# Kernel optimization log

Hardware: AMD Instinct MI355X
Metric: run time of the kernel (lower is better)

## Reference

```python
import jax, jax.numpy as jnp
import numpy as np

EPS = 1e-5  # torch LayerNorm default

def _ln(x):
    # LayerNorm over last dim, no affine (elementwise_affine=False)
    m = jnp.mean(x, axis=-1, keepdims=True)
    v = jnp.var(x, axis=-1, keepdims=True)
    return (x - m) / jnp.sqrt(v + EPS)

def _build_orthogonal(phi):
    """Orthogonal matrix of the 'X' RBS circuit on d qubits (unary subspace).
    phi has 2d-3 angles: a descending diagonal of d-1 adjacent Givens rotations
    followed by an ascending diagonal of d-2. Each RBS(theta) acts on coords
    (k, k+1) as [[cos, sin], [-sin, cos]]."""
    d = (phi.shape[0] + 3) // 2
    W = jnp.eye(d, dtype=phi.dtype)
    wires = list(range(d - 1)) + list(range(d - 3, -1, -1))  # 2d-3 gates
    for g, k in enumerate(wires):
        c, s = jnp.cos(phi[g]), jnp.sin(phi[g])
        rk, rk1 = W[k], W[k + 1]
        W = W.at[k].set(c * rk + s * rk1)
        W = W.at[k + 1].set(-s * rk + c * rk1)
    return W

def setup_inputs() -> dict:
    key = jax.random.key(0)
    ks = jax.random.split(key, 8)
    B, N, E, H, dh = 16, 1024, 512, 8, 64
    return {
        "x": jax.random.normal(ks[0], (B, N, E), jnp.float32),
        "Wv": jax.random.normal(ks[1], (H, dh, dh), jnp.float32) / np.sqrt(dh).astype(np.float32),
        "bv": jnp.zeros((H, dh), jnp.float32),
        "phi": jax.random.uniform(ks[2], (H, 2 * dh - 3), jnp.float32, 0.0, 2.0 * np.pi),
        "W1": jax.random.normal(ks[3], (E, E), jnp.float32) / np.sqrt(E).astype(np.float32),
        "b1": jnp.zeros((E,), jnp.float32),
        "W2": jax.random.normal(ks[4], (E, E), jnp.float32) / np.sqrt(E).astype(np.float32),
        "b2": jnp.zeros((E,), jnp.float32),
    }

def reference(x, Wv, bv, phi, W1, b1, W2, b2):
    B, N, E = x.shape
    H = Wv.shape[0]
    dh = E // H
    xn = _ln(x)                                    # norm1
    xh = xn.reshape(B, N, H, dh)                   # per-head slices
    Worth = jax.vmap(_build_orthogonal)(phi)       # [H, dh, dh]
    # per-head value projection (nn.Linear weights stored as [in, out])
    V = jnp.einsum('bnhd,hde->bnhe', xh, Wv) + bv  # [B,N,H,dh]
    # quantum attention scores: loader(x_j) -> W(phi) -> inverse loader(x_i),
    # rescaled by |x_i||x_j|  ==  A_ij = x_i^T W(phi) x_j
    A = jnp.einsum('bnhd,hde,bmhe->bhnm', xh, Worth, xh)
    P = jax.nn.softmax(A / np.float32(np.sqrt(dh)), axis=-1)
    attn = jnp.einsum('bhnm,bmhe->bnhe', P, V)
    head_out = _ln(attn + xh)                      # per-head LN over dh
    res = head_out.reshape(B, N, E) + x            # MHA + residual
    # merger: Linear -> GELU(exact) -> Linear on norm2(res)
    h = jax.nn.gelu(_ln(res) @ W1 + b1, approximate=False) @ W2 + b2
    return h + res
```

## Files before the change

### kernel.cpp

```cpp
#include <hip/hip_runtime.h>
#include <hip/hip_bf16.h>
#include <math.h>

#define B_  16
#define N_  1024
#define E_  512
#define H_  8

typedef __attribute__((ext_vector_type(8)))  __bf16 bf16x8;
typedef __attribute__((ext_vector_type(4)))  float  f32x4;
typedef __attribute__((ext_vector_type(16))) float  f32x16;
typedef __attribute__((ext_vector_type(4)))  unsigned int u32x4;

struct alignas(16) bf8pack { __hip_bfloat16 v[8]; };
struct alignas(8)  bf4pack { __hip_bfloat16 v[4]; };

static __device__ __forceinline__ float bf2f(__hip_bfloat16 x) { return __bfloat162float(x); }
static __device__ __forceinline__ __hip_bfloat16 f2bf(float x) { return __float2bfloat16(x); }

static __device__ __forceinline__ unsigned pkbf(float lo, float hi) {
    unsigned r;
    asm("v_cvt_pk_bf16_f32 %0, %1, %2" : "=v"(r) : "v"(lo), "v"(hi));
    return r;
}
static __device__ __forceinline__ void swap32(unsigned &a, unsigned &b) {
    asm("v_permlane32_swap_b32 %0, %1" : "+v"(a), "+v"(b));
}
static __device__ __forceinline__ void gload16(const __hip_bfloat16* g, __hip_bfloat16* l) {
    __builtin_amdgcn_global_load_lds(
        (const __attribute__((address_space(1))) unsigned*)g,
        (__attribute__((address_space(3))) unsigned*)l, 16, 0, 0);
}
#define MFMA32(a, b, c) __builtin_amdgcn_mfma_f32_32x32x16_bf16((a), (b), (c), 0, 0, 0)
#define MFMA16(a, b, c) __builtin_amdgcn_mfma_f32_16x16x32_bf16((a), (b), (c), 0, 0, 0)

static __device__ __forceinline__ float gelu_f(float v) {
    float z = fabsf(v) * 0.70710678118654752f;
    float t = 1.0f / fmaf(0.3275911f, z, 1.0f);
    float p = t * fmaf(t, fmaf(t, fmaf(t, fmaf(t, 1.061405429f, -1.453152027f),
                                       1.421413741f), -0.284496736f), 0.254829592f);
    float e = __builtin_amdgcn_exp2f(-z * z * 1.4426950408889634f);
    float erf = 1.0f - p * e;
    erf = copysignf(erf, v);
    return 0.5f * v * (1.0f + erf);
}

__global__ __launch_bounds__(256) void k_prep(const float* __restrict__ phi,
                                              const float* __restrict__ Wv,
                                              const float* __restrict__ W1,
                                              const float* __restrict__ W2,
                                              __hip_bfloat16* __restrict__ worth_t,
                                              __hip_bfloat16* __restrict__ wvt,
                                              __hip_bfloat16* __restrict__ w1t,
                                              __hip_bfloat16* __restrict__ w2t,
                                              float* __restrict__ csum1) {
    __shared__ float sh[64 * 65];
    int tid = threadIdx.x;
    if (blockIdx.x < 128) {
        int bid = blockIdx.x;
        const float* src = (bid & 1) ? W2 : W1;
        __hip_bfloat16* dst = (bid & 1) ? w2t : w1t;
        int tile = bid >> 1;
        int i0 = (tile & 7) * 64, o0 = (tile >> 3) * 64;
        float (*ts)[65] = (float(*)[65])sh;
        int r = tid >> 4, c4 = (tid & 15) * 4;
#pragma unroll
        for (int j4 = 0; j4 < 4; ++j4) {
            float4 v = *reinterpret_cast<const float4*>(&src[(size_t)(i0 + r + 16 * j4) * 512 + o0 + c4]);
            ts[r + 16 * j4][c4 + 0] = v.x; ts[r + 16 * j4][c4 + 1] = v.y;
            ts[r + 16 * j4][c4 + 2] = v.z; ts[r + 16 * j4][c4 + 3] = v.w;
        }
        __syncthreads();
        int o = tid >> 3, cg = tid & 7;
#pragma unroll
        for (int half = 0; half < 2; ++half) {
            int oo = o + 32 * half;
            bf8pack p;
#pragma unroll
            for (int j = 0; j < 8; ++j) p.v[j] = f2bf(ts[cg * 8 + j][oo]);
            *reinterpret_cast<bf8pack*>(&dst[(size_t)(o0 + oo) * 512 + i0 + cg * 8]) = p;
        }
    } else if (blockIdx.x < 136) {
        const float SCL = 0.18033688011112042f;
        int h = blockIdx.x - 128;
        int t = tid;
        if (t < 64) {
            for (int i = 0; i < 64; ++i) sh[i * 65 + t] = (i == t) ? 1.0f : 0.0f;
            for (int g = 0; g < 125; ++g) {
                int k = (g < 63) ? g : (124 - g);
                float ph = phi[h * 125 + g];
                float c, s;
                __sincosf(ph, &s, &c);
                float a  = sh[k * 65 + t];
                float b  = sh[(k + 1) * 65 + t];
                sh[k * 65 + t]       =  c * a + s * b;
                sh[(k + 1) * 65 + t] = -s * a + c * b;
            }
            for (int d = 0; d < 64; ++d)
                worth_t[h * 4096 + t * 64 + d] = f2bf(sh[d * 65 + t] * SCL);
            for (int d = 0; d < 64; ++d)
                wvt[h * 4096 + t * 64 + d] = f2bf(Wv[h * 4096 + d * 64 + t]);
        }
    } else {
        int c0 = (blockIdx.x - 136) * 64;
        float (*acc)[68] = (float(*)[68])sh;
        int cg = (tid & 15) * 4, rg = tid >> 4;
        float4 s4 = {0.f, 0.f, 0.f, 0.f};
        for (int rr = 0; rr < 32; ++rr) {
            float4 v = *reinterpret_cast<const float4*>(&W1[(size_t)(rg * 32 + rr) * 512 + c0 + cg]);
            s4.x += v.x; s4.y += v.y; s4.z += v.z; s4.w += v.w;
        }
        acc[rg][cg + 0] = s4.x; acc[rg][cg + 1] = s4.y;
        acc[rg][cg + 2] = s4.z; acc[rg][cg + 3] = s4.w;
        __syncthreads();
        if (tid < 64) {
            float s = 0.f;
#pragma unroll
            for (int g = 0; g < 16; ++g) s += acc[g][tid];
            csum1[c0 + tid] = s;
        }
    }
}

__global__ __launch_bounds__(256) void k_ln1(const float* __restrict__ in,
                                             __hip_bfloat16* __restrict__ out,
                                             __hip_bfloat16* __restrict__ outx) {
    int w = threadIdx.x >> 6, l = threadIdx.x & 63;
    size_t row = (size_t)blockIdx.x * 4 + w;
    const float* p = in + row * 512 + l * 8;
    float4 v0 = *reinterpret_cast<const float4*>(p);
    float4 v1 = *reinterpret_cast<const float4*>(p + 4);
    float vv[8] = {v0.x, v0.y, v0.z, v0.w, v1.x, v1.y, v1.z, v1.w};
    bf8pack xo;
#pragma unroll
    for (int j = 0; j < 8; ++j) xo.v[j] = f2bf(vv[j]);
    *reinterpret_cast<bf8pack*>(outx + row * 512 + l * 8) = xo;
    float s = 0.f, sq = 0.f;
#pragma unroll
    for (int j = 0; j < 8; ++j) { s += vv[j]; sq += vv[j] * vv[j]; }
#pragma unroll
    for (int o = 32; o >= 1; o >>= 1) { s += __shfl_xor(s, o); sq += __shfl_xor(sq, o); }
    float mean = s * (1.0f / 512.0f);
    float var  = sq * (1.0f / 512.0f) - mean * mean;
    float rstd = rsqrtf(var + 1e-5f);
    bf8pack ob;
#pragma unroll
    for (int j = 0; j < 8; ++j) ob.v[j] = f2bf((vv[j] - mean) * rstd);
    *reinterpret_cast<bf8pack*>(out + row * 512 + l * 8) = ob;
}

__global__ __launch_bounds__(256) void k_rowstat(const __hip_bfloat16* __restrict__ res,
                                                 float2* __restrict__ rs) {
    int w = threadIdx.x >> 6, l = threadIdx.x & 63;
    size_t row = (size_t)blockIdx.x * 4 + w;
    bf16x8 u = *reinterpret_cast<const bf16x8*>(res + row * 512 + l * 8);
    float s = 0.f, sq = 0.f;
#pragma unroll
    for (int j = 0; j < 8; ++j) { float a = (float)u[j]; s += a; sq = fmaf(a, a, sq); }
#pragma unroll
    for (int o = 32; o >= 1; o >>= 1) { s += __shfl_xor(s, o); sq += __shfl_xor(sq, o); }
    float mean = s * (1.0f / 512.0f);
    float var  = sq * (1.0f / 512.0f) - mean * mean;
    float rstd = rsqrtf(var + 1e-5f);
    if (l == 0) rs[row] = make_float2(rstd, mean * rstd);
}

__global__ __launch_bounds__(256) void k_proj(const __hip_bfloat16* __restrict__ xn,
                                              const __hip_bfloat16* __restrict__ worth_t,
                                              const __hip_bfloat16* __restrict__ wvt,
                                              const float* __restrict__ bv,
                                              __hip_bfloat16* __restrict__ xw,
                                              __hip_bfloat16* __restrict__ vt) {
    int h = blockIdx.y, rt = blockIdx.x;
    int tid = threadIdx.x, w = tid >> 6, l = tid & 63;
    int lr = l & 15, lg = l >> 4;
    int nw = rt * 64 + w * 16;
    int b  = (rt * 64) >> 10;
    int n0 = (rt * 64) & 1023;
    size_t bh = (size_t)b * H_ + h;

    __shared__ __hip_bfloat16 xw_l[64 * 72];
    __shared__ __hip_bfloat16 vt_l[64 * 72];

    const __hip_bfloat16* xp = xn + (size_t)(nw + lr) * 512 + h * 64 + lg * 8;
    bf16x8 xf0 = *reinterpret_cast<const bf16x8*>(xp);
    bf16x8 xf1 = *reinterpret_cast<const bf16x8*>(xp + 32);

    f32x4 accw[4] = {}, accv[4] = {};
#pragma unroll
    for (int g = 0; g < 4; ++g) {
        const __hip_bfloat16* wp = worth_t + h * 4096 + (g * 16 + lr) * 64 + lg * 8;
        accw[g] = MFMA16(*reinterpret_cast<const bf16x8*>(wp), xf0, accw[g]);
        accw[g] = MFMA16(*reinterpret_cast<const bf16x8*>(wp + 32), xf1, accw[g]);
        const __hip_bfloat16* vp = wvt + h * 4096 + (g * 16 + lr) * 64 + lg * 8;
        accv[g] = MFMA16(xf0, *reinterpret_cast<const bf16x8*>(vp), accv[g]);
        accv[g] = MFMA16(xf1, *reinterpret_cast<const bf16x8*>(vp + 32), accv[g]);
    }
#pragma unroll
    for (int g = 0; g < 4; ++g) {
        bf4pack pw;
#pragma unroll
        for (int r = 0; r < 4; ++r) pw.v[r] = f2bf(accw[g][r]);
        *reinterpret_cast<bf4pack*>(&xw_l[(w * 16 + lr) * 72 + g * 16 + lg * 4]) = pw;
        float bb = bv[h * 64 + g * 16 + lr];
        bf4pack pv;
#pragma unroll
        for (int r = 0; r < 4; ++r) pv.v[r] = f2bf(accv[g][r] + bb);
        *reinterpret_cast<bf4pack*>(&vt_l[(g * 16 + lr) * 72 + w * 16 + lg * 4]) = pv;
    }
    __syncthreads();
    {
        int rr = tid >> 2, c0 = (tid & 3) * 16;
        bf8pack p0 = *reinterpret_cast<const bf8pack*>(&xw_l[rr * 72 + c0]);
        bf8pack p1 = *reinterpret_cast<const bf8pack*>(&xw_l[rr * 72 + c0 + 8]);
        __hip_bfloat16* d1 = xw + (bh * N_ + n0 + rr) * 64 + c0;
        *reinterpret_cast<bf8pack*>(d1)     = p0;
        *reinterpret_cast<bf8pack*>(d1 + 8) = p1;
        bf8pack q0 = *reinterpret_cast<const bf8pack*>(&vt_l[rr * 72 + c0]);
        bf8pack q1 = *reinterpret_cast<const bf8pack*>(&vt_l[rr * 72 + c0 + 8]);
        __hip_bfloat16* d2 = vt + (bh * 64 + rr) * N_ + n0 + c0;
        *reinterpret_cast<bf8pack*>(d2)     = q0;
        *reinterpret_cast<bf8pack*>(d2 + 8) = q1;
    }
}

__global__ __launch_bounds__(512, 4) void k_attn(const __hip_bfloat16* __restrict__ xn,
                                                 const __hip_bfloat16* __restrict__ xw,
                                                 const __hip_bfloat16* __restrict__ vt,
                                                 const __hip_bfloat16* __restrict__ xb,
                                                 __hip_bfloat16* __restrict__ res) {
    int h = blockIdx.x, b = blockIdx.z;
    int tid = threadIdx.x;
    int w = tid >> 6, l = tid & 63;
    int lq = l & 31, hi = l >> 5;
    int q0 = blockIdx.y * 256 + w * 32;
    size_t bh = (size_t)b * H_ + h;

    __shared__ __hip_bfloat16 kb[2][128 * 64];
    __shared__ __hip_bfloat16 vb[2][64 * 128];
    __shared__ float lred[8][32];

    int krow = w * 16 + (l >> 3);
    const __hip_bfloat16* ksrc = xn + ((size_t)b * N_ + krow) * 512 + h * 64
                               + (((l & 7) ^ (krow & 7)) << 3);
    int vrow0 = w * 8 + (l >> 4);
    int vrow1 = vrow0 + 4;
    const __hip_bfloat16* vsrc0 = vt + (bh * 64 + vrow0) * N_ + (((l & 15) ^ (vrow0 & 15)) << 3);
    const __hip_bfloat16* vsrc1 = vt + (bh * 64 + vrow1) * N_ + (((l & 15) ^ (vrow1 & 15)) << 3);

#define STAGE(t) do { int bf_ = (t) & 1; \
        gload16(ksrc + (size_t)((t) * 128) * 512,     &kb[bf_][(w * 16) * 64]); \
        gload16(ksrc + (size_t)((t) * 128 + 8) * 512, &kb[bf_][(w * 16 + 8) * 64]); \
        gload16(vsrc0 + (t) * 128, &vb[bf_][(w * 8) * 128]); \
        gload16(vsrc1 + (t) * 128, &vb[bf_][(w * 8 + 4) * 128]); } while (0)
#define TILE_BAR() do { \
        asm volatile("s_waitcnt vmcnt(0)" ::: "memory"); \
        __builtin_amdgcn_s_barrier(); \
        __builtin_amdgcn_sched_barrier(0); } while (0)

    const __hip_bfloat16* qp = xw + (bh * N_ + q0 + lq) * 64 + 8 * hi;
    bf16x8 qf0 = *reinterpret_cast<const bf16x8*>(qp);
    bf16x8 qf1 = *reinterpret_cast<const bf16x8*>(qp + 16);
    bf16x8 qf2 = *reinterpret_cast<const bf16x8*>(qp + 32);
    bf16x8 qf3 = *reinterpret_cast<const bf16x8*>(qp + 48);

    f32x16 o0 = {}, o1 = {};
    float l_run = 0.f;
    int kso = lq & 7;
    int vso = lq & 15;

    auto body = [&](int bf_, int mm) {
        const __hip_bfloat16* kc = &kb[bf_][mm * 64 * 64];
        const __hip_bfloat16* vc = &vb[bf_][0];
        f32x16 s0 = {}, s1 = {};
        __builtin_amdgcn_s_setprio(1);
#pragma unroll
        for (int kd = 0; kd < 4; ++kd) {
            bf16x8 qf = (kd == 0) ? qf0 : (kd == 1) ? qf1 : (kd == 2) ? qf2 : qf3;
            int sl = ((kd * 2 + hi) ^ kso) << 3;
            bf16x8 ka0 = *reinterpret_cast<const bf16x8*>(kc + lq * 64 + sl);
            bf16x8 ka1 = *reinterpret_cast<const bf16x8*>(kc + (lq + 32) * 64 + sl);
            s0 = MFMA32(ka0, qf, s0);
            s1 = MFMA32(ka1, qf, s1);
        }
        __builtin_amdgcn_s_setprio(0);
#pragma unroll
        for (int i = 0; i < 16; ++i) {
            s0[i] = __builtin_amdgcn_exp2f(s0[i]);
            s1[i] = __builtin_amdgcn_exp2f(s1[i]);
        }
        float ls = 0.f;
#pragma unroll
        for (int i = 0; i < 16; ++i) ls += s0[i] + s1[i];
        l_run += ls;
        bf16x8 pa[4];
        {
            unsigned u0 = pkbf(s0[0], s0[1]), u1 = pkbf(s0[2], s0[3]);
            unsigned u2 = pkbf(s0[4], s0[5]), u3 = pkbf(s0[6], s0[7]);
            swap32(u0, u2); swap32(u1, u3);
            u32x4 uu = {u0, u1, u2, u3};
            pa[0] = __builtin_bit_cast(bf16x8, uu);
        }
        {
            unsigned u0 = pkbf(s0[8], s0[9]),   u1 = pkbf(s0[10], s0[11]);
            unsigned u2 = pkbf(s0[12], s0[13]), u3 = pkbf(s0[14], s0[15]);
            swap32(u0, u2); swap32(u1, u3);
            u32x4 uu = {u0, u1, u2, u3};
            pa[1] = __builtin_bit_cast(bf16x8, uu);
        }
        {
            unsigned u0 = pkbf(s1[0], s1[1]), u1 = pkbf(s1[2], s1[3]);
            unsigned u2 = pkbf(s1[4], s1[5]), u3 = pkbf(s1[6], s1[7]);
            swap32(u0, u2); swap32(u1, u3);
            u32x4 uu = {u0, u1, u2, u3};
            pa[2] = __builtin_bit_cast(bf16x8, uu);
        }
        {
            unsigned u0 = pkbf(s1[8], s1[9]),   u1 = pkbf(s1[10], s1[11]);
            unsigned u2 = pkbf(s1[12], s1[13]), u3 = pkbf(s1[14], s1[15]);
            swap32(u0, u2); swap32(u1, u3);
            u32x4 uu = {u0, u1, u2, u3};
            pa[3] = __builtin_bit_cast(bf16x8, uu);
        }
        __builtin_amdgcn_s_setprio(1);
#pragma unroll
        for (int ks = 0; ks < 4; ++ks) {
            int sl = ((mm * 8 + ks * 2 + hi) ^ vso) << 3;
            bf16x8 v0 = *reinterpret_cast<const bf16x8*>(vc + lq * 128 + sl);
            bf16x8 v1 = *reinterpret_cast<const bf16x8*>(vc + (lq + 32) * 128 + sl);
            o0 = MFMA32(pa[ks], v0, o0);
            o1 = MFMA32(pa[ks], v1, o1);
        }
        __builtin_amdgcn_s_setprio(0);
    };

    STAGE(0);
    TILE_BAR();
    for (int t = 0; t < 7; ++t) {
        STAGE(t + 1);
        body(t & 1, 0);
        body(t & 1, 1);
        TILE_BAR();
    }
    body(1, 0);
    body(1, 1);

    float lt = l_run + __shfl_xor(l_run, 32);
    if (hi == 0) lred[w][lq] = 1.0f / lt;
#pragma unroll
    for (int r = 0; r < 16; ++r) {
        int qr = (r & 3) + 8 * (r >> 2) + 4 * hi;
        float li = lred[w][qr];
        size_t base = ((size_t)b * N_ + q0 + qr) * 512 + h * 64;
        float t0 = o0[r] * li + bf2f(xn[base + lq]);
        float t1 = o1[r] * li + bf2f(xn[base + 32 + lq]);
        float s1v = t0 + t1, s2v = t0 * t0 + t1 * t1;
#pragma unroll
        for (int off = 16; off >= 1; off >>= 1) { s1v += __shfl_xor(s1v, off); s2v += __shfl_xor(s2v, off); }
        float mean = s1v * (1.0f / 64.0f);
        float var  = s2v * (1.0f / 64.0f) - mean * mean;
        float rstd = rsqrtf(var + 1e-5f);
        res[base + lq]      = f2bf((t0 - mean) * rstd + bf2f(xb[base + lq]));
        res[base + 32 + lq] = f2bf((t1 - mean) * rstd + bf2f(xb[base + 32 + lq]));
    }
#undef STAGE
#undef TILE_BAR
}

template <int MODE>
__global__ __launch_bounds__(256, 5) void k_gemm(const __hip_bfloat16* __restrict__ A,
                                                 const __hip_bfloat16* __restrict__ Bt,
                                                 const float* __restrict__ bias,
                                                 const __hip_bfloat16* __restrict__ resid,
                                                 const float2* __restrict__ rstat,
                                                 const float* __restrict__ csum,
                                                 __hip_bfloat16* __restrict__ outb,
                                                 float* __restrict__ outf) {
    int m0 = blockIdx.x * 128, nn0 = blockIdx.y * 64;
    int tid = threadIdx.x, w = tid >> 6, l = tid & 63;
    int lr = l & 15, lg = l >> 4;
    __shared__ __hip_bfloat16 bs[2][64 * 128];

    int srow = w * 16 + (l >> 4);
    int sslot = l & 15;

#define GSTAGE(c) do { \
        _Pragma("unroll") \
        for (int i_ = 0; i_ < 4; ++i_) { \
            int row_ = srow + i_ * 4; \
            gload16(Bt + (size_t)(nn0 + row_) * 512 + (c) * 128 + ((sslot ^ (row_ & 15)) << 3), \
                    &bs[(c) & 1][(w * 16 + i_ * 4) * 128]); \
        } } while (0)

    GSTAGE(0);
    asm volatile("s_waitcnt vmcnt(0)" ::: "memory");
    __builtin_amdgcn_s_barrier();
    __builtin_amdgcn_sched_barrier(0);

    f32x4 acc0[4] = {}, acc1[4] = {};
    const __hip_bfloat16* ap0 = A + (size_t)(m0 + w * 32 + lr) * 512 + lg * 8;
    const __hip_bfloat16* ap1 = ap0 + 16 * 512;
#pragma unroll
    for (int c = 0; c < 4; ++c) {
        if (c < 3) GSTAGE(c + 1);
        const __hip_bfloat16* bc = &bs[c & 1][0];
#pragma unroll
        for (int kk = 0; kk < 4; ++kk) {
            bf16x8 a0 = *reinterpret_cast<const bf16x8*>(ap0 + c * 128 + kk * 32);
            bf16x8 a1 = *reinterpret_cast<const bf16x8*>(ap1 + c * 128 + kk * 32);
#pragma unroll
            for (int g = 0; g < 4; ++g) {
                int row = g * 16 + lr;
                bf16x8 bf = *reinterpret_cast<const bf16x8*>(
                    bc + row * 128 + (((kk * 4 + lg) ^ (row & 15)) << 3));
                acc0[g] = MFMA16(a0, bf, acc0[g]);
                acc1[g] = MFMA16(a1, bf, acc1[g]);
            }
        }
        if (c < 3) {
            asm volatile("s_waitcnt vmcnt(0)" ::: "memory");
            __builtin_amdgcn_s_barrier();
            __builtin_amdgcn_sched_barrier(0);
        }
    }
#undef GSTAGE
    float2 rsA[4], rsB[4];
    if (MODE == 0) {
#pragma unroll
        for (int r = 0; r < 4; ++r) {
            rsA[r] = rstat[m0 + w * 32 + lg * 4 + r];
            rsB[r] = rstat[m0 + w * 32 + lg * 4 + r + 16];
        }
    }
#pragma unroll
    for (int g = 0; g < 4; ++g) {
        int col = nn0 + g * 16 + lr;
        float bb = bias[col];
        float cc = (MODE == 0) ? csum[col] : 0.f;
#pragma unroll
        for (int r = 0; r < 4; ++r) {
            int row0 = m0 + w * 32 + lg * 4 + r;
            if (MODE == 0) {
                float v0 = fmaf(acc0[g][r], rsA[r].x, fmaf(-rsA[r].y, cc, bb));
                float v1 = fmaf(acc1[g][r], rsB[r].x, fmaf(-rsB[r].y, cc, bb));
                outb[(size_t)row0 * 512 + col] = f2bf(gelu_f(v0));
                outb[(size_t)(row0 + 16) * 512 + col] = f2bf(gelu_f(v1));
            } else {
                size_t i0 = (size_t)row0 * 512 + col;
                size_t i1 = (size_t)(row0 + 16) * 512 + col;
                outf[i0] = acc0[g][r] + bb + bf2f(resid[i0]);
                outf[i1] = acc1[g][r] + bb + bf2f(resid[i1]);
            }
        }
    }
}

extern "C" void kernel_launch(void* const* d_in, const int* in_sizes, int n_in,
                              void* d_out, int out_size, void* d_ws, size_t ws_size,
                              hipStream_t stream) {
    const float* x   = (const float*)d_in[0];
    const float* Wv  = (const float*)d_in[1];
    const float* bv  = (const float*)d_in[2];
    const float* phi = (const float*)d_in[3];
    const float* W1  = (const float*)d_in[4];
    const float* b1  = (const float*)d_in[5];
    const float* W2  = (const float*)d_in[6];
    const float* b2  = (const float*)d_in[7];
    float* out = (float*)d_out;

    char* ws = (char*)d_ws;
    __hip_bfloat16* worth_t = (__hip_bfloat16*)(ws + 0);
    __hip_bfloat16* wvt     = (__hip_bfloat16*)(ws + 65536);
    __hip_bfloat16* w1t     = (__hip_bfloat16*)(ws + 131072);
    __hip_bfloat16* w2t     = (__hip_bfloat16*)(ws + 655360);
    float*          csum1   = (float*)(ws + 1179648);
    float2*         rstat   = (float2*)(ws + 1181696);
    __hip_bfloat16* xn      = (__hip_bfloat16*)(ws + 1312768);
    __hip_bfloat16* xw      = (__hip_bfloat16*)(ws + 18089984);
    __hip_bfloat16* vt      = (__hip_bfloat16*)(ws + 34867200);
    __hip_bfloat16* res     = (__hip_bfloat16*)(ws + 51644416);
    __hip_bfloat16* y1      = (__hip_bfloat16*)(ws + 68421632);
    __hip_bfloat16* xb      = (__hip_bfloat16*)(ws + 85198848);

    k_prep<<<dim3(144), dim3(256), 0, stream>>>(phi, Wv, W1, W2, worth_t, wvt, w1t, w2t, csum1);
    k_ln1<<<dim3(4096), dim3(256), 0, stream>>>(x, xn, xb);
    k_proj<<<dim3(256, 8), dim3(256), 0, stream>>>(xn, worth_t, wvt, bv, xw, vt);
    k_attn<<<dim3(8, 4, 16), dim3(512), 0, stream>>>(xn, xw, vt, xb, res);
    k_rowstat<<<dim3(4096), dim3(256), 0, stream>>>(res, rstat);
    k_gemm<0><<<dim3(128, 8), dim3(256), 0, stream>>>(res, w1t, b1, nullptr, rstat, csum1, y1, nullptr);
    k_gemm<1><<<dim3(128, 8), dim3(256), 0, stream>>>(y1, w2t, b2, res, nullptr, nullptr, nullptr, out);
}
```

Measured before the change: 155.8 us.

## Shrink attention blocks to 4 waves with 64-key tiles per stage

The attention kernel goes from 512-thread blocks covering 256 queries to 256-thread blocks covering 128 queries, which doubles the grid. The K/V staging tiles shrink from 128 to 64 keys, and the loop runs 16 single-body iterations instead of 8 double-body ones. LDS use per block drops so more blocks can be resident and the grid fills the GPU better. In exchange, every K/V tile is loaded from global memory by twice as many blocks, and a barrier is paid for each smaller tile.

New measurement: 158.3 us. About the same (+1.6%).

```diff
diff --git a/kernel.cpp b/kernel.cpp
--- a/kernel.cpp
+++ b/kernel.cpp
@@ -224,7 +224,7 @@
     }
 }
 
-__global__ __launch_bounds__(512, 4) void k_attn(const __hip_bfloat16* __restrict__ xn,
+__global__ __launch_bounds__(256, 4) void k_attn(const __hip_bfloat16* __restrict__ xn,
                                                  const __hip_bfloat16* __restrict__ xw,
                                                  const __hip_bfloat16* __restrict__ vt,
                                                  const __hip_bfloat16* __restrict__ xb,
@@ -233,26 +233,24 @@
     int tid = threadIdx.x;
     int w = tid >> 6, l = tid & 63;
     int lq = l & 31, hi = l >> 5;
-    int q0 = blockIdx.y * 256 + w * 32;
+    int so = lq & 7;
+    int q0 = blockIdx.y * 128 + w * 32;
     size_t bh = (size_t)b * H_ + h;
 
-    __shared__ __hip_bfloat16 kb[2][128 * 64];
-    __shared__ __hip_bfloat16 vb[2][64 * 128];
-    __shared__ float lred[8][32];
-
-    int krow = w * 16 + (l >> 3);
-    const __hip_bfloat16* ksrc = xn + ((size_t)b * N_ + krow) * 512 + h * 64
-                               + (((l & 7) ^ (krow & 7)) << 3);
-    int vrow0 = w * 8 + (l >> 4);
-    int vrow1 = vrow0 + 4;
-    const __hip_bfloat16* vsrc0 = vt + (bh * 64 + vrow0) * N_ + (((l & 15) ^ (vrow0 & 15)) << 3);
-    const __hip_bfloat16* vsrc1 = vt + (bh * 64 + vrow1) * N_ + (((l & 15) ^ (vrow1 & 15)) << 3);
+    __shared__ __hip_bfloat16 kb[2][4096];
+    __shared__ __hip_bfloat16 vb[2][4096];
+    __shared__ float lred[4][32];
+
+    int rloc = w * 16 + (l >> 3);
+    int gs = ((l & 7) ^ (rloc & 7)) << 3;
+    const __hip_bfloat16* ksrc = xn + ((size_t)b * N_ + rloc) * 512 + h * 64 + gs;
+    const __hip_bfloat16* vsrc = vt + (bh * 64 + rloc) * N_ + gs;
 
 #define STAGE(t) do { int bf_ = (t) & 1; \
-        gload16(ksrc + (size_t)((t) * 128) * 512,     &kb[bf_][(w * 16) * 64]); \
-        gload16(ksrc + (size_t)((t) * 128 + 8) * 512, &kb[bf_][(w * 16 + 8) * 64]); \
-        gload16(vsrc0 + (t) * 128, &vb[bf_][(w * 8) * 128]); \
-        gload16(vsrc1 + (t) * 128, &vb[bf_][(w * 8 + 4) * 128]); } while (0)
+        gload16(ksrc + (size_t)((t) * 64) * 512,       &kb[bf_][(w * 16) * 64]); \
+        gload16(ksrc + (size_t)((t) * 64 + 8) * 512,   &kb[bf_][(w * 16 + 8) * 64]); \
+        gload16(vsrc + (t) * 64,                       &vb[bf_][(w * 16) * 64]); \
+        gload16(vsrc + (t) * 64 + 8 * N_,              &vb[bf_][(w * 16 + 8) * 64]); } while (0)
 #define TILE_BAR() do { \
         asm volatile("s_waitcnt vmcnt(0)" ::: "memory"); \
         __builtin_amdgcn_s_barrier(); \
@@ -266,18 +264,16 @@
 
     f32x16 o0 = {}, o1 = {};
     float l_run = 0.f;
-    int kso = lq & 7;
-    int vso = lq & 15;
-
-    auto body = [&](int bf_, int mm) {
-        const __hip_bfloat16* kc = &kb[bf_][mm * 64 * 64];
+
+    auto body = [&](int bf_) {
+        const __hip_bfloat16* kc = &kb[bf_][0];
         const __hip_bfloat16* vc = &vb[bf_][0];
         f32x16 s0 = {}, s1 = {};
         __builtin_amdgcn_s_setprio(1);
 #pragma unroll
         for (int kd = 0; kd < 4; ++kd) {
             bf16x8 qf = (kd == 0) ? qf0 : (kd == 1) ? qf1 : (kd == 2) ? qf2 : qf3;
-            int sl = ((kd * 2 + hi) ^ kso) << 3;
+            int sl = ((kd * 2 + hi) ^ so) << 3;
             bf16x8 ka0 = *reinterpret_cast<const bf16x8*>(kc + lq * 64 + sl);
             bf16x8 ka1 = *reinterpret_cast<const bf16x8*>(kc + (lq + 32) * 64 + sl);
             s0 = MFMA32(ka0, qf, s0);
@@ -325,9 +321,9 @@
         __builtin_amdgcn_s_setprio(1);
 #pragma unroll
         for (int ks = 0; ks < 4; ++ks) {
-            int sl = ((mm * 8 + ks * 2 + hi) ^ vso) << 3;
-            bf16x8 v0 = *reinterpret_cast<const bf16x8*>(vc + lq * 128 + sl);
-            bf16x8 v1 = *reinterpret_cast<const bf16x8*>(vc + (lq + 32) * 128 + sl);
+            int sl = ((ks * 2 + hi) ^ so) << 3;
+            bf16x8 v0 = *reinterpret_cast<const bf16x8*>(vc + lq * 64 + sl);
+            bf16x8 v1 = *reinterpret_cast<const bf16x8*>(vc + (lq + 32) * 64 + sl);
             o0 = MFMA32(pa[ks], v0, o0);
             o1 = MFMA32(pa[ks], v1, o1);
         }
@@ -336,14 +332,12 @@
 
     STAGE(0);
     TILE_BAR();
-    for (int t = 0; t < 7; ++t) {
+    for (int t = 0; t < 15; ++t) {
         STAGE(t + 1);
-        body(t & 1, 0);
-        body(t & 1, 1);
+        body(t & 1);
         TILE_BAR();
     }
-    body(1, 0);
-    body(1, 1);
+    body(1);
 
     float lt = l_run + __shfl_xor(l_run, 32);
     if (hi == 0) lred[w][lq] = 1.0f / lt;
@@ -485,7 +479,7 @@
     k_prep<<<dim3(144), dim3(256), 0, stream>>>(phi, Wv, W1, W2, worth_t, wvt, w1t, w2t, csum1);
     k_ln1<<<dim3(4096), dim3(256), 0, stream>>>(x, xn, xb);
     k_proj<<<dim3(256, 8), dim3(256), 0, stream>>>(xn, worth_t, wvt, bv, xw, vt);
-    k_attn<<<dim3(8, 4, 16), dim3(512), 0, stream>>>(xn, xw, vt, xb, res);
+    k_attn<<<dim3(8, 8, 16), dim3(256), 0, stream>>>(xn, xw, vt, xb, res);
     k_rowstat<<<dim3(4096), dim3(256), 0, stream>>>(res, rstat);
     k_gemm<0><<<dim3(128, 8), dim3(256), 0, stream>>>(res, w1t, b1, nullptr, rstat, csum1, y1, nullptr);
     k_gemm<1><<<dim3(128, 8), dim3(256), 0, stream>>>(y1, w2t, b2, res, nullptr, nullptr, nullptr, out);
```
